# Optimization experiments

Measured on AMD Instinct MI355X. Metric: run time of the kernel, lower is better.

The kernel has to match this reference:

```python
import jax, jax.numpy as jnp
import numpy as np

B, N, D, H = 8, 2048, 256, 8
HD = D // H  # head_dim = 32
LN_EPS = 1e-5


def setup_inputs() -> dict:
    key = jax.random.key(0)
    ks = jax.random.split(key, 8)
    x = jax.random.normal(ks[0], (B, N, D), dtype=jnp.float32)
    # dense 0/1 adjacency with guaranteed self-loops (avoids all -inf softmax rows)
    adj = jax.random.randint(ks[1], (B, N, N), 0, 2, dtype=jnp.int32)
    adj = jnp.maximum(adj, jnp.eye(N, dtype=jnp.int32)[None, :, :])
    s = 0.02
    Wq = jax.random.normal(ks[2], (D, D), dtype=jnp.float32) * s
    Wk = jax.random.normal(ks[3], (D, D), dtype=jnp.float32) * s
    Wv = jax.random.normal(ks[4], (D, D), dtype=jnp.float32) * s
    Wo = jax.random.normal(ks[5], (D, D), dtype=jnp.float32) * s
    zeros = jnp.zeros((D,), dtype=jnp.float32)
    return {
        "x": x, "adjacency": adj,
        "Wq": Wq, "bq": zeros, "Wk": Wk, "bk": zeros,
        "Wv": Wv, "bv": zeros, "Wo": Wo, "bo": zeros,
        "gamma": jnp.ones((D,), dtype=jnp.float32), "beta": zeros,
    }


def reference(x, adjacency, Wq, bq, Wk, bk, Wv, bv, Wo, bo, gamma, beta):
    b, n, d = x.shape
    q = (x @ Wq + bq).reshape(b, n, H, HD)
    k = (x @ Wk + bk).reshape(b, n, H, HD)
    v = (x @ Wv + bv).reshape(b, n, H, HD)
    # scores: [B, N(query), M(key), H]
    scores = jnp.einsum('bnhd,bmhd->bnmh', q, k) / jnp.sqrt(jnp.float32(HD))
    mask = (adjacency == 0)[..., None]  # [B,N,M,1] broadcasts over heads
    scores = jnp.where(mask, -jnp.inf, scores)
    weights = jax.nn.softmax(scores, axis=2)  # softmax over key axis m
    # dropout is identity in eval mode
    attended = jnp.einsum('bnmh,bmhd->bnhd', weights, v).reshape(b, n, d)
    out = attended @ Wo + bo
    out = out + x  # residual (output.shape == x.shape since input_dim == output_dim)
    mu = jnp.mean(out, axis=-1, keepdims=True)
    var = jnp.mean(jnp.square(out - mu), axis=-1, keepdims=True)
    return (out - mu) * jax.lax.rsqrt(var + LN_EPS) * gamma + beta
```

## Files before the change

### kernel.cpp

```cpp
#include <hip/hip_runtime.h>
#include <hip/hip_bf16.h>
#include <cstdint>
#include <cstddef>

#define B_ 8
#define N_ 2048
#define D_ 256
#define H_ 8
#define HD_ 32
#define LN_EPS 1e-5f
#define QSCALE 0.25506275f

typedef __attribute__((ext_vector_type(8))) short short8;
typedef __attribute__((ext_vector_type(4))) float f32x4;
typedef __attribute__((ext_vector_type(16))) float f32x16;

static __device__ __forceinline__ float exp2v(float x) {
#if __has_builtin(__builtin_amdgcn_exp2f)
    return __builtin_amdgcn_exp2f(x);
#else
    float r;
    asm("v_exp_f32 %0, %1" : "=v"(r) : "v"(x));
    return r;
#endif
}

static __device__ __forceinline__ unsigned short f2bf(float f) {
    union { float f; unsigned int u; } v; v.f = f;
    unsigned int r = v.u + 0x7fffu + ((v.u >> 16) & 1u);
    return (unsigned short)(r >> 16);
}

static __device__ __forceinline__ unsigned int cvtpk(float lo, float hi) {
    unsigned int d;
    asm("v_cvt_pk_bf16_f32 %0, %1, %2" : "=v"(d) : "v"(lo), "v"(hi));
    return d;
}

__global__ __launch_bounds__(256) void k_prep_w(const float* __restrict__ w0, const float* __restrict__ w1,
                                                const float* __restrict__ w2, const float* __restrict__ w3,
                                                unsigned short* __restrict__ wt) {
    int c = blockIdx.x, mat = blockIdx.y, k = threadIdx.x;
    const float* w = (mat == 0) ? w0 : (mat == 1) ? w1 : (mat == 2) ? w2 : w3;
    wt[((size_t)(mat * 256 + c)) * 256 + k] = f2bf(w[k * 256 + c]);
}

__global__ __launch_bounds__(256) void k_mask(const int* __restrict__ adj,
                                              unsigned int* __restrict__ mbg) {
    int wave = (blockIdx.x * 256 + threadIdx.x) >> 6;
    int lane = threadIdx.x & 63;
    int shamt = 4 * (lane & 7);
    int g8 = lane >> 3;
    const int4* p = reinterpret_cast<const int4*>(adj) + (size_t)wave * 512 + lane;
    unsigned int* outp = mbg + (size_t)wave * 64;

    int4 v[8];
#pragma unroll
    for (int i = 0; i < 8; ++i)
        v[i] = p[i * 64];
    __builtin_amdgcn_sched_barrier(0);

#pragma unroll
    for (int i = 0; i < 8; ++i) {
        unsigned int nib = (v[i].x != 0 ? 1u : 0u) | (v[i].y != 0 ? 2u : 0u)
                         | (v[i].z != 0 ? 4u : 0u) | (v[i].w != 0 ? 8u : 0u);
        unsigned int r = nib << shamt;
        r |= (unsigned int)__shfl_xor((int)r, 1, 64);
        r |= (unsigned int)__shfl_xor((int)r, 2, 64);
        r |= (unsigned int)__shfl_xor((int)r, 4, 64);
        if ((lane & 7) == 0) outp[i * 8 + g8] = r;
    }
}

__global__ __launch_bounds__(256) void k_maskT2(const unsigned int* __restrict__ mbg,
                                                unsigned int* __restrict__ mbgT2) {
    __shared__ unsigned int bits[64][65];
    int tid = threadIdx.x, lane = tid & 63, wv = tid >> 6;
    int b = blockIdx.x >> 5, qg = blockIdx.x & 31;

    {
        int row = tid >> 2, cc = (tid & 3) * 16;
        const uint4* src = reinterpret_cast<const uint4*>(
            mbg + ((size_t)(b * N_ + qg * 64 + row)) * 64 + cc);
#pragma unroll
        for (int j = 0; j < 4; ++j) {
            uint4 v = src[j];
            bits[row][cc + 4 * j + 0] = v.x; bits[row][cc + 4 * j + 1] = v.y;
            bits[row][cc + 4 * j + 2] = v.z; bits[row][cc + 4 * j + 3] = v.w;
        }
    }
    __syncthreads();

    int h = lane >> 5, l31 = lane & 31;
    const unsigned int M[5] = {0x0000FFFFu, 0x00FF00FFu, 0x0F0F0F0Fu, 0x33333333u, 0x55555555u};
#pragma unroll
    for (int j = 0; j < 16; ++j) {
        int kw = wv * 16 + j;
        unsigned int w = bits[lane][kw];
#pragma unroll
        for (int si = 0; si < 5; ++si) {
            int s = 16 >> si;
            unsigned int m = M[si];
            unsigned int t = (unsigned int)__shfl_xor((int)w, s, 64);
            unsigned int a = (w & m) | ((t & m) << s);
            unsigned int c = (w & ~m) | ((t >> s) & m);
            w = (lane & s) ? c : a;
        }
        int k = kw * 32 + l31;
        int kp = (k & ~7) | ((k & 3) << 1) | ((k >> 2) & 1);
        mbgT2[((size_t)(b * 64 + qg * 2 + h)) * 2048 + kp] = w;
    }
}

__global__ __launch_bounds__(256) void k_qkv(const float* __restrict__ x,
                                             const unsigned short* __restrict__ wt,
                                             const float* __restrict__ bq, const float* __restrict__ bk,
                                             const float* __restrict__ bv,
                                             unsigned short* __restrict__ Qb, unsigned short* __restrict__ Kb,
                                             unsigned short* __restrict__ Vs) {
    int lane = threadIdx.x & 63;
    int wv = threadIdx.x >> 6;
    int row0 = blockIdx.x * 64 + wv * 16;
    int l15 = lane & 15, lg = lane >> 4;

    short8 af[8];
    const float* xrow = x + (size_t)(row0 + l15) * 256 + lg * 8;
#pragma unroll
    for (int kk = 0; kk < 8; ++kk) {
        float4 a = *reinterpret_cast<const float4*>(xrow + kk * 32);
        float4 b = *reinterpret_cast<const float4*>(xrow + kk * 32 + 4);
        union { short8 s8; unsigned int u[4]; } t;
        t.u[0] = cvtpk(a.x, a.y); t.u[1] = cvtpk(a.z, a.w);
        t.u[2] = cvtpk(b.x, b.y); t.u[3] = cvtpk(b.z, b.w);
        af[kk] = t.s8;
    }

    int b = row0 >> 11;
    int nbase = (row0 & 2047) + lg * 4;

#pragma unroll 1
    for (int mat = 0; mat < 3; ++mat) {
        const float* bias = (mat == 0) ? bq : (mat == 1) ? bk : bv;
        const float qs = (mat == 0) ? QSCALE : 1.0f;
        const unsigned short* wm = wt + (size_t)mat * 65536;
        for (int ci = 0; ci < 16; ++ci) {
            const unsigned short* wrow = wm + (size_t)(ci * 16 + l15) * 256 + lg * 8;
            f32x4 acc = {0.f, 0.f, 0.f, 0.f};
#pragma unroll
            for (int kk = 0; kk < 8; ++kk) {
                short8 bfg = *reinterpret_cast<const short8*>(wrow + kk * 32);
                acc = __builtin_amdgcn_mfma_f32_16x16x32_bf16(af[kk], bfg, acc, 0, 0, 0);
            }
            int col = ci * 16 + l15;
            float bcol = bias[col];
            int h = col >> 5, hd = col & 31;
            if (mat < 2) {
                unsigned short* dst = (mat == 0) ? Qb : Kb;
#pragma unroll
                for (int r = 0; r < 4; ++r) {
                    size_t off = ((size_t)(b * 8 + h) * 2048 + nbase + r) * 32 + hd;
                    dst[off] = f2bf((acc[r] + bcol) * qs);
                }
            } else {
                size_t off = (size_t)(b * 8 + h) * 65536
                           + ((size_t)(nbase >> 4) * 32 + hd) * 16 + (nbase & 15);
                ushort4 o;
                o.x = f2bf(acc[0] + bcol); o.y = f2bf(acc[1] + bcol);
                o.z = f2bf(acc[2] + bcol); o.w = f2bf(acc[3] + bcol);
                *reinterpret_cast<ushort4*>(Vs + off) = o;
            }
        }
    }
}

#define SL(j, offs) asm("s_load_dwordx2 %0, %1, " offs : "=s"(m##j) : "s"(mbase))
#define SLOAD16() do { \
    SL(0, "0x0");  SL(1, "0x8");  SL(2, "0x10"); SL(3, "0x18"); \
    SL(4, "0x20"); SL(5, "0x28"); SL(6, "0x30"); SL(7, "0x38"); \
    SL(8, "0x40"); SL(9, "0x48"); SL(10, "0x50"); SL(11, "0x58"); \
    SL(12, "0x60"); SL(13, "0x68"); SL(14, "0x70"); SL(15, "0x78"); } while (0)
#define CND(d, s_, mj) asm("v_cndmask_b32 %0, 0, %1, %2" : "=v"(d) : "v"(s_), "s"(mj))

__global__ __launch_bounds__(256, 6) void k_attn(const unsigned short* __restrict__ Qb,
                                                 const unsigned short* __restrict__ Kb,
                                                 const unsigned short* __restrict__ Vs,
                                                 const unsigned int* __restrict__ mbgT2,
                                                 unsigned short* __restrict__ att) {
    int tid = threadIdx.x;
    int lane = tid & 63;
    int l31 = lane & 31, hi = lane >> 5;
    int b = blockIdx.x & 7;
    int hg = (blockIdx.x >> 3) & 1;
    int qt32 = blockIdx.x >> 4;
    int q0 = qt32 * 32;
    int head = hg * 4 + (tid >> 6);
    int bh = b * 8 + head;

    const unsigned short* Qh = Qb + (size_t)bh * N_ * HD_;
    const unsigned short* Kh = Kb + (size_t)bh * N_ * HD_;
    const unsigned short* Vh = Vs + (size_t)bh * 65536;

    short8 qf0 = *reinterpret_cast<const short8*>(Qh + (size_t)(q0 + l31) * HD_ + hi * 8);
    short8 qf1 = *reinterpret_cast<const short8*>(Qh + (size_t)(q0 + l31) * HD_ + hi * 8 + 16);
    const unsigned short* krow = Kh + (size_t)l31 * HD_ + hi * 8;
    const unsigned short* vfp = Vh + (size_t)l31 * 16 + hi * 8;

    unsigned long long mbase = (unsigned long long)(mbgT2 + (size_t)(b * 64 + qt32) * 2048);
    unsigned long long m0, m1, m2, m3, m4, m5, m6, m7, m8, m9, m10, m11, m12, m13, m14, m15;
    SLOAD16();

    const f32x16 fz = {0.f,0.f,0.f,0.f,0.f,0.f,0.f,0.f,0.f,0.f,0.f,0.f,0.f,0.f,0.f,0.f};
    const short8 onesf = {0x3F80, 0x3F80, 0x3F80, 0x3F80, 0x3F80, 0x3F80, 0x3F80, 0x3F80};
    f32x16 attacc = fz;
    f32x16 onesacc = fz;

#pragma unroll 2
    for (int t = 0; t < 64; ++t) {
        short8 kf0 = *reinterpret_cast<const short8*>(krow + (size_t)t * 1024);
        short8 kf1 = *reinterpret_cast<const short8*>(krow + (size_t)t * 1024 + 16);
        short8 vf0 = *reinterpret_cast<const short8*>(vfp + (size_t)t * 1024);
        short8 vf1 = *reinterpret_cast<const short8*>(vfp + (size_t)t * 1024 + 512);

        __builtin_amdgcn_s_setprio(1);
        f32x16 s = __builtin_amdgcn_mfma_f32_32x32x16_bf16(kf0, qf0, fz, 0, 0, 0);
        s = __builtin_amdgcn_mfma_f32_32x32x16_bf16(kf1, qf1, s, 0, 0, 0);
        __builtin_amdgcn_s_setprio(0);

        float e0 = exp2v(s[0]),  e1 = exp2v(s[1]),  e2 = exp2v(s[2]),  e3 = exp2v(s[3]);
        float e4 = exp2v(s[4]),  e5 = exp2v(s[5]),  e6 = exp2v(s[6]),  e7 = exp2v(s[7]);
        float e8 = exp2v(s[8]),  e9 = exp2v(s[9]),  e10 = exp2v(s[10]), e11 = exp2v(s[11]);
        float e12 = exp2v(s[12]), e13 = exp2v(s[13]), e14 = exp2v(s[14]), e15 = exp2v(s[15]);

        asm volatile("s_waitcnt lgkmcnt(0)"
                     : "+s"(m0), "+s"(m1), "+s"(m2), "+s"(m3), "+s"(m4), "+s"(m5), "+s"(m6), "+s"(m7),
                       "+s"(m8), "+s"(m9), "+s"(m10), "+s"(m11), "+s"(m12), "+s"(m13), "+s"(m14), "+s"(m15));

        float p0, p1, p2, p3, p4, p5, p6, p7, p8, p9, p10, p11, p12, p13, p14, p15;
        CND(p0, e0, m0);   CND(p1, e1, m1);   CND(p2, e2, m2);   CND(p3, e3, m3);
        CND(p4, e4, m4);   CND(p5, e5, m5);   CND(p6, e6, m6);   CND(p7, e7, m7);
        CND(p8, e8, m8);   CND(p9, e9, m9);   CND(p10, e10, m10); CND(p11, e11, m11);
        CND(p12, e12, m12); CND(p13, e13, m13); CND(p14, e14, m14); CND(p15, e15, m15);

        unsigned int pd[4][2];
        pd[0][0] = cvtpk(p0, p1);   pd[0][1] = cvtpk(p2, p3);
        pd[1][0] = cvtpk(p4, p5);   pd[1][1] = cvtpk(p6, p7);
        pd[2][0] = cvtpk(p8, p9);   pd[2][1] = cvtpk(p10, p11);
        pd[3][0] = cvtpk(p12, p13); pd[3][1] = cvtpk(p14, p15);

        mbase += 128;
        SLOAD16();

        asm("v_permlane32_swap_b32 %0, %1" : "+v"(pd[0][0]), "+v"(pd[1][0]));
        asm("v_permlane32_swap_b32 %0, %1" : "+v"(pd[0][1]), "+v"(pd[1][1]));
        asm("v_permlane32_swap_b32 %0, %1" : "+v"(pd[2][0]), "+v"(pd[3][0]));
        asm("v_permlane32_swap_b32 %0, %1" : "+v"(pd[2][1]), "+v"(pd[3][1]));

        union { short8 s8; unsigned int u[4]; } bf0, bf1;
        bf0.u[0] = pd[0][0]; bf0.u[1] = pd[0][1]; bf0.u[2] = pd[1][0]; bf0.u[3] = pd[1][1];
        bf1.u[0] = pd[2][0]; bf1.u[1] = pd[2][1]; bf1.u[2] = pd[3][0]; bf1.u[3] = pd[3][1];

        __builtin_amdgcn_s_setprio(1);
        attacc = __builtin_amdgcn_mfma_f32_32x32x16_bf16(vf0, bf0.s8, attacc, 0, 0, 0);
        attacc = __builtin_amdgcn_mfma_f32_32x32x16_bf16(vf1, bf1.s8, attacc, 0, 0, 0);
        onesacc = __builtin_amdgcn_mfma_f32_32x32x16_bf16(onesf, bf0.s8, onesacc, 0, 0, 0);
        onesacc = __builtin_amdgcn_mfma_f32_32x32x16_bf16(onesf, bf1.s8, onesacc, 0, 0, 0);
        __builtin_amdgcn_s_setprio(0);
    }

    float rcp = 1.f / onesacc[0];

    unsigned short* arow = att + ((size_t)b * N_ + q0 + l31) * D_ + head * HD_;
#pragma unroll
    for (int g = 0; g < 4; ++g) {
        ushort4 o;
        o.x = f2bf(attacc[4 * g + 0] * rcp);
        o.y = f2bf(attacc[4 * g + 1] * rcp);
        o.z = f2bf(attacc[4 * g + 2] * rcp);
        o.w = f2bf(attacc[4 * g + 3] * rcp);
        *reinterpret_cast<ushort4*>(arow + 8 * g + 4 * hi) = o;
    }
}

__global__ __launch_bounds__(256) void k_outln(const unsigned short* __restrict__ att,
                                               const unsigned short* __restrict__ wot,
                                               const float* __restrict__ bo,
                                               const float* __restrict__ x,
                                               const float* __restrict__ gamma, const float* __restrict__ beta,
                                               float* __restrict__ out) {
    int lane = threadIdx.x & 63, wv = threadIdx.x >> 6;
    int l15 = lane & 15, lg = lane >> 4;
    int row0 = blockIdx.x * 64 + wv * 16;

    short8 af[8];
    const unsigned short* arow = att + (size_t)(row0 + l15) * 256 + lg * 8;
#pragma unroll
    for (int kk = 0; kk < 8; ++kk)
        af[kk] = *reinterpret_cast<const short8*>(arow + kk * 32);

    float v[16][4];
#pragma unroll
    for (int ci = 0; ci < 16; ++ci) {
        const unsigned short* wrow = wot + (size_t)(ci * 16 + l15) * 256 + lg * 8;
        f32x4 acc = {0.f, 0.f, 0.f, 0.f};
#pragma unroll
        for (int kk = 0; kk < 8; ++kk) {
            short8 bfg = *reinterpret_cast<const short8*>(wrow + kk * 32);
            acc = __builtin_amdgcn_mfma_f32_16x16x32_bf16(af[kk], bfg, acc, 0, 0, 0);
        }
        float bcol = bo[ci * 16 + l15];
#pragma unroll
        for (int r = 0; r < 4; ++r)
            v[ci][r] = acc[r] + bcol + x[(size_t)(row0 + lg * 4 + r) * 256 + ci * 16 + l15];
    }

    float sum[4] = {0.f, 0.f, 0.f, 0.f}, sq[4] = {0.f, 0.f, 0.f, 0.f};
#pragma unroll
    for (int ci = 0; ci < 16; ++ci)
#pragma unroll
        for (int r = 0; r < 4; ++r) {
            sum[r] += v[ci][r];
            sq[r] += v[ci][r] * v[ci][r];
        }
#pragma unroll
    for (int d = 1; d < 16; d <<= 1)
#pragma unroll
        for (int r = 0; r < 4; ++r) {
            sum[r] += __shfl_xor(sum[r], d, 64);
            sq[r] += __shfl_xor(sq[r], d, 64);
        }

    float mu[4], rs[4];
#pragma unroll
    for (int r = 0; r < 4; ++r) {
        mu[r] = sum[r] * (1.f / 256.f);
        float var = sq[r] * (1.f / 256.f) - mu[r] * mu[r];
        rs[r] = rsqrtf(var + LN_EPS);
    }

#pragma unroll
    for (int ci = 0; ci < 16; ++ci) {
        float g = gamma[ci * 16 + l15], be = beta[ci * 16 + l15];
#pragma unroll
        for (int r = 0; r < 4; ++r)
            out[(size_t)(row0 + lg * 4 + r) * 256 + ci * 16 + l15] = (v[ci][r] - mu[r]) * rs[r] * g + be;
    }
}

extern "C" void kernel_launch(void* const* d_in, const int* in_sizes, int n_in,
                              void* d_out, int out_size, void* d_ws, size_t ws_size,
                              hipStream_t stream) {
    (void)in_sizes; (void)n_in; (void)out_size; (void)ws_size;
    const float* x     = (const float*)d_in[0];
    const int*   adj   = (const int*)d_in[1];
    const float* Wq    = (const float*)d_in[2];
    const float* bq    = (const float*)d_in[3];
    const float* Wk    = (const float*)d_in[4];
    const float* bk    = (const float*)d_in[5];
    const float* Wv    = (const float*)d_in[6];
    const float* bv    = (const float*)d_in[7];
    const float* Wo    = (const float*)d_in[8];
    const float* bo    = (const float*)d_in[9];
    const float* gamma = (const float*)d_in[10];
    const float* beta  = (const float*)d_in[11];
    float* out = (float*)d_out;

    char* ws = (char*)d_ws;
    unsigned short* wt   = (unsigned short*)ws; ws += (size_t)4 * 256 * 256 * 2;
    unsigned short* Qb   = (unsigned short*)ws; ws += (size_t)B_ * H_ * N_ * HD_ * 2;
    unsigned short* Kb   = (unsigned short*)ws; ws += (size_t)B_ * H_ * N_ * HD_ * 2;
    unsigned short* Vs   = (unsigned short*)ws; ws += (size_t)B_ * H_ * N_ * HD_ * 2;
    unsigned short* att  = (unsigned short*)ws; ws += (size_t)16384 * 256 * 2;
    unsigned int*   mbg  = (unsigned int*)ws;   ws += (size_t)B_ * N_ * 64 * 4;
    unsigned int*   mbgT2 = (unsigned int*)ws;  ws += (size_t)B_ * 64 * 2048 * 4 + 256;

    k_prep_w<<<dim3(256, 4), 256, 0, stream>>>(Wq, Wk, Wv, Wo, wt);
    k_mask<<<4096, 256, 0, stream>>>(adj, mbg);
    k_maskT2<<<256, 256, 0, stream>>>(mbg, mbgT2);
    k_qkv<<<256, 256, 0, stream>>>(x, wt, bq, bk, bv, Qb, Kb, Vs);
    k_attn<<<1024, 256, 0, stream>>>(Qb, Kb, Vs, mbgT2, att);
    k_outln<<<256, 256, 0, stream>>>(att, wt + 3 * 65536, bo, x, gamma, beta, out);
}
```

Before: 183.3 us.

## Software-pipeline QK scores in attention and split QKV projection across grid

```diff
diff --git a/kernel.cpp b/kernel.cpp
--- a/kernel.cpp
+++ b/kernel.cpp
@@ -118,10 +118,14 @@
                                              const float* __restrict__ bv,
                                              unsigned short* __restrict__ Qb, unsigned short* __restrict__ Kb,
                                              unsigned short* __restrict__ Vs) {
+    int mat = blockIdx.y;
     int lane = threadIdx.x & 63;
     int wv = threadIdx.x >> 6;
     int row0 = blockIdx.x * 64 + wv * 16;
     int l15 = lane & 15, lg = lane >> 4;
+    const float* bias = (mat == 0) ? bq : (mat == 1) ? bk : bv;
+    const float qs = (mat == 0) ? QSCALE : 1.0f;
+    const unsigned short* wm = wt + (size_t)mat * 65536;
 
     short8 af[8];
     const float* xrow = x + (size_t)(row0 + l15) * 256 + lg * 8;
@@ -138,37 +142,31 @@
     int b = row0 >> 11;
     int nbase = (row0 & 2047) + lg * 4;
 
-#pragma unroll 1
-    for (int mat = 0; mat < 3; ++mat) {
-        const float* bias = (mat == 0) ? bq : (mat == 1) ? bk : bv;
-        const float qs = (mat == 0) ? QSCALE : 1.0f;
-        const unsigned short* wm = wt + (size_t)mat * 65536;
-        for (int ci = 0; ci < 16; ++ci) {
-            const unsigned short* wrow = wm + (size_t)(ci * 16 + l15) * 256 + lg * 8;
-            f32x4 acc = {0.f, 0.f, 0.f, 0.f};
-#pragma unroll
-            for (int kk = 0; kk < 8; ++kk) {
-                short8 bfg = *reinterpret_cast<const short8*>(wrow + kk * 32);
-                acc = __builtin_amdgcn_mfma_f32_16x16x32_bf16(af[kk], bfg, acc, 0, 0, 0);
+    for (int ci = 0; ci < 16; ++ci) {
+        const unsigned short* wrow = wm + (size_t)(ci * 16 + l15) * 256 + lg * 8;
+        f32x4 acc = {0.f, 0.f, 0.f, 0.f};
+#pragma unroll
+        for (int kk = 0; kk < 8; ++kk) {
+            short8 bfg = *reinterpret_cast<const short8*>(wrow + kk * 32);
+            acc = __builtin_amdgcn_mfma_f32_16x16x32_bf16(af[kk], bfg, acc, 0, 0, 0);
+        }
+        int col = ci * 16 + l15;
+        float bcol = bias[col];
+        int h = col >> 5, hd = col & 31;
+        if (mat < 2) {
+            unsigned short* dst = (mat == 0) ? Qb : Kb;
+#pragma unroll
+            for (int r = 0; r < 4; ++r) {
+                size_t off = ((size_t)(b * 8 + h) * 2048 + nbase + r) * 32 + hd;
+                dst[off] = f2bf((acc[r] + bcol) * qs);
             }
-            int col = ci * 16 + l15;
-            float bcol = bias[col];
-            int h = col >> 5, hd = col & 31;
-            if (mat < 2) {
-                unsigned short* dst = (mat == 0) ? Qb : Kb;
-#pragma unroll
-                for (int r = 0; r < 4; ++r) {
-                    size_t off = ((size_t)(b * 8 + h) * 2048 + nbase + r) * 32 + hd;
-                    dst[off] = f2bf((acc[r] + bcol) * qs);
-                }
-            } else {
-                size_t off = (size_t)(b * 8 + h) * 65536
-                           + ((size_t)(nbase >> 4) * 32 + hd) * 16 + (nbase & 15);
-                ushort4 o;
-                o.x = f2bf(acc[0] + bcol); o.y = f2bf(acc[1] + bcol);
-                o.z = f2bf(acc[2] + bcol); o.w = f2bf(acc[3] + bcol);
-                *reinterpret_cast<ushort4*>(Vs + off) = o;
-            }
+        } else {
+            size_t off = (size_t)(b * 8 + h) * 65536
+                       + ((size_t)(nbase >> 4) * 32 + hd) * 16 + (nbase & 15);
+            ushort4 o;
+            o.x = f2bf(acc[0] + bcol); o.y = f2bf(acc[1] + bcol);
+            o.z = f2bf(acc[2] + bcol); o.w = f2bf(acc[3] + bcol);
+            *reinterpret_cast<ushort4*>(Vs + off) = o;
         }
     }
 }
@@ -181,7 +179,7 @@
     SL(12, "0x60"); SL(13, "0x68"); SL(14, "0x70"); SL(15, "0x78"); } while (0)
 #define CND(d, s_, mj) asm("v_cndmask_b32 %0, 0, %1, %2" : "=v"(d) : "v"(s_), "s"(mj))
 
-__global__ __launch_bounds__(256, 6) void k_attn(const unsigned short* __restrict__ Qb,
+__global__ __launch_bounds__(256, 4) void k_attn(const unsigned short* __restrict__ Qb,
                                                  const unsigned short* __restrict__ Kb,
                                                  const unsigned short* __restrict__ Vs,
                                                  const unsigned int* __restrict__ mbgT2,
@@ -214,22 +212,31 @@
     f32x16 attacc = fz;
     f32x16 onesacc = fz;
 
-#pragma unroll 2
+    short8 kA0 = *reinterpret_cast<const short8*>(krow);
+    short8 kA1 = *reinterpret_cast<const short8*>(krow + 16);
+    f32x16 sC = __builtin_amdgcn_mfma_f32_32x32x16_bf16(kA0, qf0, fz, 0, 0, 0);
+    sC = __builtin_amdgcn_mfma_f32_32x32x16_bf16(kA1, qf1, sC, 0, 0, 0);
+    kA0 = *reinterpret_cast<const short8*>(krow + 1024);
+    kA1 = *reinterpret_cast<const short8*>(krow + 1024 + 16);
+
+#pragma unroll 1
     for (int t = 0; t < 64; ++t) {
-        short8 kf0 = *reinterpret_cast<const short8*>(krow + (size_t)t * 1024);
-        short8 kf1 = *reinterpret_cast<const short8*>(krow + (size_t)t * 1024 + 16);
+        int tk = (t + 2 < 64) ? t + 2 : 63;
+        short8 kN0 = *reinterpret_cast<const short8*>(krow + (size_t)tk * 1024);
+        short8 kN1 = *reinterpret_cast<const short8*>(krow + (size_t)tk * 1024 + 16);
         short8 vf0 = *reinterpret_cast<const short8*>(vfp + (size_t)t * 1024);
         short8 vf1 = *reinterpret_cast<const short8*>(vfp + (size_t)t * 1024 + 512);
 
         __builtin_amdgcn_s_setprio(1);
-        f32x16 s = __builtin_amdgcn_mfma_f32_32x32x16_bf16(kf0, qf0, fz, 0, 0, 0);
-        s = __builtin_amdgcn_mfma_f32_32x32x16_bf16(kf1, qf1, s, 0, 0, 0);
+        f32x16 sN = __builtin_amdgcn_mfma_f32_32x32x16_bf16(kA0, qf0, fz, 0, 0, 0);
+        sN = __builtin_amdgcn_mfma_f32_32x32x16_bf16(kA1, qf1, sN, 0, 0, 0);
         __builtin_amdgcn_s_setprio(0);
-
-        float e0 = exp2v(s[0]),  e1 = exp2v(s[1]),  e2 = exp2v(s[2]),  e3 = exp2v(s[3]);
-        float e4 = exp2v(s[4]),  e5 = exp2v(s[5]),  e6 = exp2v(s[6]),  e7 = exp2v(s[7]);
-        float e8 = exp2v(s[8]),  e9 = exp2v(s[9]),  e10 = exp2v(s[10]), e11 = exp2v(s[11]);
-        float e12 = exp2v(s[12]), e13 = exp2v(s[13]), e14 = exp2v(s[14]), e15 = exp2v(s[15]);
+        __builtin_amdgcn_sched_barrier(0);
+
+        float e0 = exp2v(sC[0]),  e1 = exp2v(sC[1]),  e2 = exp2v(sC[2]),  e3 = exp2v(sC[3]);
+        float e4 = exp2v(sC[4]),  e5 = exp2v(sC[5]),  e6 = exp2v(sC[6]),  e7 = exp2v(sC[7]);
+        float e8 = exp2v(sC[8]),  e9 = exp2v(sC[9]),  e10 = exp2v(sC[10]), e11 = exp2v(sC[11]);
+        float e12 = exp2v(sC[12]), e13 = exp2v(sC[13]), e14 = exp2v(sC[14]), e15 = exp2v(sC[15]);
 
         asm volatile("s_waitcnt lgkmcnt(0)"
                      : "+s"(m0), "+s"(m1), "+s"(m2), "+s"(m3), "+s"(m4), "+s"(m5), "+s"(m6), "+s"(m7),
@@ -265,6 +272,8 @@
         onesacc = __builtin_amdgcn_mfma_f32_32x32x16_bf16(onesf, bf0.s8, onesacc, 0, 0, 0);
         onesacc = __builtin_amdgcn_mfma_f32_32x32x16_bf16(onesf, bf1.s8, onesacc, 0, 0, 0);
         __builtin_amdgcn_s_setprio(0);
+
+        sC = sN; kA0 = kN0; kA1 = kN1;
     }
 
     float rcp = 1.f / onesacc[0];
@@ -371,12 +380,12 @@
     unsigned short* Vs   = (unsigned short*)ws; ws += (size_t)B_ * H_ * N_ * HD_ * 2;
     unsigned short* att  = (unsigned short*)ws; ws += (size_t)16384 * 256 * 2;
     unsigned int*   mbg  = (unsigned int*)ws;   ws += (size_t)B_ * N_ * 64 * 4;
-    unsigned int*   mbgT2 = (unsigned int*)ws;  ws += (size_t)B_ * 64 * 2048 * 4 + 256;
+    unsigned int*   mbgT2 = (unsigned int*)ws;  ws += (size_t)B_ * 64 * 2048 * 4 + 8192;
 
     k_prep_w<<<dim3(256, 4), 256, 0, stream>>>(Wq, Wk, Wv, Wo, wt);
     k_mask<<<4096, 256, 0, stream>>>(adj, mbg);
     k_maskT2<<<256, 256, 0, stream>>>(mbg, mbgT2);
-    k_qkv<<<256, 256, 0, stream>>>(x, wt, bq, bk, bv, Qb, Kb, Vs);
+    k_qkv<<<dim3(256, 3), 256, 0, stream>>>(x, wt, bq, bk, bv, Qb, Kb, Vs);
     k_attn<<<1024, 256, 0, stream>>>(Qb, Kb, Vs, mbgT2, att);
     k_outln<<<256, 256, 0, stream>>>(att, wt + 3 * 65536, bo, x, gamma, beta, out);
 }
```

Result: slower. 190.7 us (+4.1%).
